# Kernel tuning notes

Hardware: AMD Instinct MI355X
Metric: run time of the kernel (lower is better)

The kernel has to match this reference:

```python
import jax, jax.numpy as jnp
import numpy as np

D = 768
HEAD_DIM = 64
NHEADS = D // HEAD_DIM
B, S = 2, 4096


def setup_inputs() -> dict:
    key = jax.random.key(0)
    ks = jax.random.split(key, 9)
    std = 1.0 / np.sqrt(D)
    inp = {"x": jax.random.normal(ks[0], (B, S, D), dtype=jnp.float32)}
    for i, name in enumerate(["Wq", "Wk", "Wv", "Wo"]):
        inp[name + "_w"] = jax.random.uniform(ks[1 + 2 * i], (D, D), dtype=jnp.float32, minval=-std, maxval=std)
        inp[name + "_b"] = jax.random.uniform(ks[2 + 2 * i], (D,), dtype=jnp.float32, minval=-std, maxval=std)
    return inp


def reference(x, Wq_w, Wq_b, Wk_w, Wk_b, Wv_w, Wv_b, Wo_w, Wo_b):
    b, s, d = x.shape
    # nn.Linear: y = x @ W.T + b
    q = x @ Wq_w.T + Wq_b
    k = x @ Wk_w.T + Wk_b
    v = x @ Wv_w.T + Wv_b
    # [B, H, S, hd]
    q = q.reshape(b, s, NHEADS, HEAD_DIM).transpose(0, 2, 1, 3)
    k = k.reshape(b, s, NHEADS, HEAD_DIM).transpose(0, 2, 1, 3)
    v = v.reshape(b, s, NHEADS, HEAD_DIM).transpose(0, 2, 1, 3)
    scale = jnp.sqrt(jnp.asarray(HEAD_DIM, dtype=q.dtype))
    logits = jnp.einsum('bhqd,bhkd->bhqk', q, k) / scale  # [B,H,S,S]
    causal_mask = jnp.triu(jnp.ones((s, s), dtype=bool), k=1)
    logits = jnp.where(causal_mask, -jnp.inf, logits)
    a = jax.nn.softmax(logits, axis=-1)
    preout = jnp.einsum('bhqk,bhkd->bhqd', a, v)
    preout = preout.transpose(0, 2, 1, 3).reshape(b, s, d)
    return preout @ Wo_w.T + Wo_b
```

## Files before the change

kernel.cpp:

```cpp
#include <hip/hip_runtime.h>

typedef unsigned short u16;
typedef unsigned int u32;
typedef __bf16 bf16_t;
typedef bf16_t bf16x8 __attribute__((ext_vector_type(8)));
typedef float f32x4 __attribute__((ext_vector_type(4)));
typedef float f32x16 __attribute__((ext_vector_type(16)));

#define DM 768
#define HD 64
#define NH 12
#define NB 2
#define SEQ 4096
#define MR (NB * SEQ)

#define SCL2E_F (0.125f * 1.44269504088896340736f)

__device__ __forceinline__ u16 f2bf(float f) {
  union { float f; u32 u; } v;
  v.f = f;
  u32 r = v.u + 0x7FFFu + ((v.u >> 16) & 1u);
  return (u16)(r >> 16);
}

__device__ __forceinline__ u32 cvtpk(float a, float b) {
  u32 r;
  asm("v_cvt_pk_bf16_f32 %0, %1, %2" : "=v"(r) : "v"(a), "v"(b));
  return r;
}

__device__ __forceinline__ bf16x8 ldb8(const u16* p) {
  return *reinterpret_cast<const bf16x8*>(p);
}

__device__ __forceinline__ f32x4 mfma16(bf16x8 a, bf16x8 b, f32x4 c) {
  return __builtin_amdgcn_mfma_f32_16x16x32_bf16(a, b, c, 0, 0, 0);
}

__device__ __forceinline__ f32x16 mfma32(bf16x8 a, bf16x8 b, f32x16 c) {
  return __builtin_amdgcn_mfma_f32_32x32x16_bf16(a, b, c, 0, 0, 0);
}

#define GLDS16(g, l)                                              \
  __builtin_amdgcn_global_load_lds(                               \
      (const __attribute__((address_space(1))) void*)(g),         \
      (__attribute__((address_space(3))) void*)(l), 16, 0, 0)

__global__ __launch_bounds__(256) void cvt_kernel(const float* __restrict__ src,
                                                  u16* __restrict__ dst, int n8) {
  int i = blockIdx.x * 256 + threadIdx.x;
  if (i >= n8) return;
  const float4* s = reinterpret_cast<const float4*>(src) + (size_t)i * 2;
  float4 a = s[0], b = s[1];
  union { u16 u[8]; uint4 v; } o;
  o.u[0] = f2bf(a.x); o.u[1] = f2bf(a.y); o.u[2] = f2bf(a.z); o.u[3] = f2bf(a.w);
  o.u[4] = f2bf(b.x); o.u[5] = f2bf(b.y); o.u[6] = f2bf(b.z); o.u[7] = f2bf(b.w);
  reinterpret_cast<uint4*>(dst)[i] = o.v;
}

__global__ __launch_bounds__(256) void cvt_w_kernel(const float* __restrict__ w0,
                                                    const float* __restrict__ w1,
                                                    const float* __restrict__ w2,
                                                    const float* __restrict__ w3,
                                                    u16* __restrict__ dst) {
  const float* src = (blockIdx.y == 0) ? w0 : (blockIdx.y == 1) ? w1
                   : (blockIdx.y == 2) ? w2 : w3;
  u16* d = dst + (size_t)blockIdx.y * DM * DM;
  int i = blockIdx.x * 256 + threadIdx.x;
  const float4* s = reinterpret_cast<const float4*>(src) + (size_t)i * 2;
  float4 a = s[0], b = s[1];
  union { u16 u[8]; uint4 v; } o;
  o.u[0] = f2bf(a.x); o.u[1] = f2bf(a.y); o.u[2] = f2bf(a.z); o.u[3] = f2bf(a.w);
  o.u[4] = f2bf(b.x); o.u[5] = f2bf(b.y); o.u[6] = f2bf(b.z); o.u[7] = f2bf(b.w);
  reinterpret_cast<uint4*>(d)[i] = o.v;
}

__global__ __launch_bounds__(256) void gemm_qkv_kernel(
    const u16* __restrict__ A, const u16* __restrict__ Wall,
    const float* __restrict__ b0, const float* __restrict__ b1,
    const float* __restrict__ b2, u16* __restrict__ O) {
  __shared__ __align__(16) u16 As[128 * 32];
  __shared__ __align__(16) u16 Bs[128 * 32];

  const int tid = threadIdx.x;
  const int w = tid >> 6, lane = tid & 63;
  const int l16 = lane & 15, lg = lane >> 4;
  const int wm = w >> 1, wn = w & 1;

  const int m0 = blockIdx.x * 128;
  const int n0 = blockIdx.y * 128;
  const int z = blockIdx.z;

  const u16* W = Wall + (size_t)z * DM * DM;
  const float* bias = (z == 0) ? b0 : ((z == 1) ? b1 : b2);
  u16* oz = O + (size_t)z * MR * DM;
  const float qscale = (z == 0) ? SCL2E_F : 1.f;

  f32x4 acc[4][4];
#pragma unroll
  for (int i = 0; i < 4; ++i)
#pragma unroll
    for (int j = 0; j < 4; ++j) {
      acc[i][j][0] = 0.f; acc[i][j][1] = 0.f;
      acc[i][j][2] = 0.f; acc[i][j][3] = 0.f;
    }

  for (int k0 = 0; k0 < DM; k0 += 32) {
#pragma unroll
    for (int i = 0; i < 2; ++i) {
      const int c = (w * 2 + i) * 64 + lane;
      const int m = c >> 2, kc = c & 3;
      GLDS16(A + (size_t)(m0 + m) * DM + (k0 + kc * 8),
             As + (size_t)(w * 2 + i) * 512);
      GLDS16(W + (size_t)(n0 + m) * DM + (k0 + kc * 8),
             Bs + (size_t)(w * 2 + i) * 512);
    }
    __syncthreads();
    bf16x8 af[4], bfv[4];
#pragma unroll
    for (int i = 0; i < 4; ++i)
      af[i] = ldb8(As + (wm * 64 + i * 16 + l16) * 32 + lg * 8);
#pragma unroll
    for (int j = 0; j < 4; ++j)
      bfv[j] = ldb8(Bs + (wn * 64 + j * 16 + l16) * 32 + lg * 8);
#pragma unroll
    for (int i = 0; i < 4; ++i)
#pragma unroll
      for (int j = 0; j < 4; ++j)
        acc[i][j] = mfma16(af[i], bfv[j], acc[i][j]);
    __syncthreads();
  }

#pragma unroll
  for (int i = 0; i < 4; ++i) {
    const int gm = m0 + wm * 64 + i * 16 + lg * 4;
    const int bb = gm >> 12;
    const int ss = gm & (SEQ - 1);
#pragma unroll
    for (int j = 0; j < 4; ++j) {
      const int gn = n0 + wn * 64 + j * 16 + l16;
      const int hh = gn >> 6, dd = gn & (HD - 1);
      const float bv = bias[gn];
      if (z == 2) {
        union { u16 u[4]; uint2 v; } pk;
#pragma unroll
        for (int r = 0; r < 4; ++r) pk.u[r] = f2bf(acc[i][j][r] + bv);
        *reinterpret_cast<uint2*>(
            oz + ((size_t)(bb * NH + hh) * HD + dd) * SEQ + ss) = pk.v;
      } else {
        u16* op = oz + ((size_t)(bb * NH + hh) * SEQ + ss) * HD + dd;
#pragma unroll
        for (int r = 0; r < 4; ++r)
          op[(size_t)r * HD] = f2bf((acc[i][j][r] + bv) * qscale);
      }
    }
  }
}

__global__ __launch_bounds__(256) void gemm_out_kernel(
    const u16* __restrict__ A, const u16* __restrict__ W,
    const float* __restrict__ bias, float* __restrict__ Out) {
  __shared__ __align__(16) u16 As[128 * 32];
  __shared__ __align__(16) u16 Bs[128 * 32];

  const int tid = threadIdx.x;
  const int w = tid >> 6, lane = tid & 63;
  const int l16 = lane & 15, lg = lane >> 4;
  const int wm = w >> 1, wn = w & 1;

  const int m0 = blockIdx.x * 128;
  const int n0 = blockIdx.y * 128;

  f32x4 acc[4][4];
#pragma unroll
  for (int i = 0; i < 4; ++i)
#pragma unroll
    for (int j = 0; j < 4; ++j) {
      acc[i][j][0] = 0.f; acc[i][j][1] = 0.f;
      acc[i][j][2] = 0.f; acc[i][j][3] = 0.f;
    }

  for (int k0 = 0; k0 < DM; k0 += 32) {
#pragma unroll
    for (int i = 0; i < 2; ++i) {
      const int c = (w * 2 + i) * 64 + lane;
      const int m = c >> 2, kc = c & 3;
      GLDS16(A + (size_t)(m0 + m) * DM + (k0 + kc * 8),
             As + (size_t)(w * 2 + i) * 512);
      GLDS16(W + (size_t)(n0 + m) * DM + (k0 + kc * 8),
             Bs + (size_t)(w * 2 + i) * 512);
    }
    __syncthreads();
    bf16x8 af[4], bfv[4];
#pragma unroll
    for (int i = 0; i < 4; ++i)
      af[i] = ldb8(As + (wm * 64 + i * 16 + l16) * 32 + lg * 8);
#pragma unroll
    for (int j = 0; j < 4; ++j)
      bfv[j] = ldb8(Bs + (wn * 64 + j * 16 + l16) * 32 + lg * 8);
#pragma unroll
    for (int i = 0; i < 4; ++i)
#pragma unroll
      for (int j = 0; j < 4; ++j)
        acc[i][j] = mfma16(af[i], bfv[j], acc[i][j]);
    __syncthreads();
  }

#pragma unroll
  for (int i = 0; i < 4; ++i) {
    const int gm = m0 + wm * 64 + i * 16 + lg * 4;
#pragma unroll
    for (int j = 0; j < 4; ++j) {
      const int gn = n0 + wn * 64 + j * 16 + l16;
      const float bv = bias[gn];
      float* op = Out + (size_t)gm * DM + gn;
#pragma unroll
      for (int r = 0; r < 4; ++r)
        op[(size_t)r * DM] = acc[i][j][r] + bv;
    }
  }
}

__global__ __launch_bounds__(256) void attn_kernel(
    const u16* __restrict__ Qg, const u16* __restrict__ Kg,
    const u16* __restrict__ VTg, u16* __restrict__ Og) {
  __shared__ __align__(16) u16 Kt[2][64][72];
  __shared__ __align__(16) u16 Vt[2][64][72];

  const int tid = threadIdx.x;
  const int w = tid >> 6, lane = tid & 63;
  const int l32 = lane & 31, hi = lane >> 5;

  const int idx = blockIdx.x;
  const int qt = 31 - (idx / 24);
  const int bh = idx % 24;
  const int bb = bh / NH, hh = bh % NH;

  const u16* Qp = Qg + (size_t)bh * SEQ * HD;
  const u16* Kp = Kg + (size_t)bh * SEQ * HD;
  const u16* VTp = VTg + (size_t)bh * HD * SEQ;

  const int qw0 = qt * 128 + w * 32;
  const int qlane = qw0 + l32;

  bf16x8 qf[4];
#pragma unroll
  for (int c = 0; c < 4; ++c)
    qf[c] = ldb8(Qp + (size_t)qlane * HD + c * 16 + hi * 8);

  f32x16 oacc[2];
#pragma unroll
  for (int db = 0; db < 2; ++db)
#pragma unroll
    for (int r = 0; r < 16; ++r) oacc[db][r] = 0.f;
  float mrun = -__builtin_inff();
  float lsum = 0.f;

  const int srow = tid >> 3;
  const int sc8 = (tid & 7) * 8;

  {
    uint4 a = *reinterpret_cast<const uint4*>(Kp + (size_t)srow * HD + sc8);
    uint4 b = *reinterpret_cast<const uint4*>(
        Kp + (size_t)(srow + 32) * HD + sc8);
    uint4 c = *reinterpret_cast<const uint4*>(
        VTp + (size_t)srow * SEQ + sc8);
    uint4 d = *reinterpret_cast<const uint4*>(
        VTp + (size_t)(srow + 32) * SEQ + sc8);
    *reinterpret_cast<uint4*>(&Kt[0][srow][sc8]) = a;
    *reinterpret_cast<uint4*>(&Kt[0][srow + 32][sc8]) = b;
    *reinterpret_cast<uint4*>(&Vt[0][srow][sc8]) = c;
    *reinterpret_cast<uint4*>(&Vt[0][srow + 32][sc8]) = d;
  }

  const int NT = 2 * qt + 2;
  int cur = 0;
  for (int t = 0; t < NT; ++t) {
    const int kv0 = t * 64;
    const bool pf = (t + 1 < NT);
    uint4 nK0, nK1, nV0, nV1;
    if (pf) {
      const int nk = kv0 + 64;
      nK0 = *reinterpret_cast<const uint4*>(
          Kp + (size_t)(nk + srow) * HD + sc8);
      nK1 = *reinterpret_cast<const uint4*>(
          Kp + (size_t)(nk + srow + 32) * HD + sc8);
      nV0 = *reinterpret_cast<const uint4*>(
          VTp + (size_t)srow * SEQ + nk + sc8);
      nV1 = *reinterpret_cast<const uint4*>(
          VTp + (size_t)(srow + 32) * SEQ + nk + sc8);
    }
    __syncthreads();

    const bool active = (kv0 <= qw0 + 31);
    f32x16 st[2];
    if (active) {
      __builtin_amdgcn_s_setprio(1);
#pragma unroll
      for (int b = 0; b < 2; ++b) {
#pragma unroll
        for (int r = 0; r < 16; ++r) st[b][r] = 0.f;
#pragma unroll
        for (int c = 0; c < 4; ++c) {
          bf16x8 kf = ldb8(&Kt[cur][b * 32 + l32][c * 16 + hi * 8]);
          st[b] = mfma32(kf, qf[c], st[b]);
        }
      }
      __builtin_amdgcn_s_setprio(0);

      if (kv0 + 63 > qw0) {
#pragma unroll
        for (int b = 0; b < 2; ++b)
#pragma unroll
          for (int r = 0; r < 16; ++r) {
            const int kvi = kv0 + b * 32 + (r & 3) + 8 * (r >> 2) + 4 * hi;
            if (kvi > qlane) st[b][r] = -__builtin_inff();
          }
      }

      float mx[8];
#pragma unroll
      for (int r = 0; r < 8; ++r)
        mx[r] = fmaxf(fmaxf(st[0][r], st[0][r + 8]),
                      fmaxf(st[1][r], st[1][r + 8]));
#pragma unroll
      for (int r = 0; r < 4; ++r) mx[r] = fmaxf(mx[r], mx[r + 4]);
      mx[0] = fmaxf(mx[0], mx[2]);
      mx[1] = fmaxf(mx[1], mx[3]);
      float mt = fmaxf(mx[0], mx[1]);
      mt = fmaxf(mt, __shfl_xor(mt, 32));

      if (__any(mt > mrun + 8.f)) {
        const float mnew = fmaxf(mrun, mt);
        const float corr = exp2f(mrun - mnew);
        lsum *= corr;
#pragma unroll
        for (int db = 0; db < 2; ++db)
#pragma unroll
          for (int r = 0; r < 16; ++r) oacc[db][r] *= corr;
        mrun = mnew;
      }

#pragma unroll
      for (int r = 0; r < 16; ++r) {
        st[0][r] = exp2f(st[0][r] - mrun);
        st[1][r] = exp2f(st[1][r] - mrun);
      }
      float sm[8];
#pragma unroll
      for (int r = 0; r < 8; ++r)
        sm[r] = (st[0][r] + st[0][r + 8]) + (st[1][r] + st[1][r + 8]);
#pragma unroll
      for (int r = 0; r < 4; ++r) sm[r] += sm[r + 4];
      lsum += (sm[0] + sm[2]) + (sm[1] + sm[3]);
    }

    if (pf) {
      *reinterpret_cast<uint4*>(&Kt[cur ^ 1][srow][sc8]) = nK0;
      *reinterpret_cast<uint4*>(&Kt[cur ^ 1][srow + 32][sc8]) = nK1;
      *reinterpret_cast<uint4*>(&Vt[cur ^ 1][srow][sc8]) = nV0;
      *reinterpret_cast<uint4*>(&Vt[cur ^ 1][srow + 32][sc8]) = nV1;
    }

    if (active) {
#pragma unroll
      for (int b = 0; b < 2; ++b) {
#pragma unroll
        for (int h = 0; h < 2; ++h) {
          u32 a0 = cvtpk(st[b][h * 8 + 0], st[b][h * 8 + 1]);
          u32 a1 = cvtpk(st[b][h * 8 + 2], st[b][h * 8 + 3]);
          u32 a2 = cvtpk(st[b][h * 8 + 4], st[b][h * 8 + 5]);
          u32 a3 = cvtpk(st[b][h * 8 + 6], st[b][h * 8 + 7]);
          const u32 p0 = (u32)__shfl_xor((int)a0, 32);
          const u32 p1 = (u32)__shfl_xor((int)a1, 32);
          const u32 p2 = (u32)__shfl_xor((int)a2, 32);
          const u32 p3 = (u32)__shfl_xor((int)a3, 32);
          union { u32 w[4]; bf16x8 v; } pb;
          pb.w[0] = hi ? p2 : a0;
          pb.w[1] = hi ? p3 : a1;
          pb.w[2] = hi ? a2 : p0;
          pb.w[3] = hi ? a3 : p1;
          const int c = 2 * b + h;
          __builtin_amdgcn_s_setprio(1);
#pragma unroll
          for (int db = 0; db < 2; ++db) {
            bf16x8 vf = ldb8(&Vt[cur][db * 32 + l32][c * 16 + hi * 8]);
            oacc[db] = mfma32(vf, pb.v, oacc[db]);
          }
          __builtin_amdgcn_s_setprio(0);
        }
      }
    }
    cur ^= 1;
  }

  const float ltot = lsum + __shfl_xor(lsum, 32);
  const float linv = 1.f / ltot;

  u16* Op = Og + ((size_t)bb * SEQ + qlane) * DM + hh * HD;
#pragma unroll
  for (int db = 0; db < 2; ++db)
#pragma unroll
    for (int r = 0; r < 16; r += 2) {
      const int d = db * 32 + (r & 3) + 8 * (r >> 2) + 4 * hi;
      u32 pk = cvtpk(oacc[db][r] * linv, oacc[db][r + 1] * linv);
      *reinterpret_cast<u32*>(Op + d) = pk;
    }
}

extern "C" void kernel_launch(void* const* d_in, const int* in_sizes, int n_in,
                              void* d_out, int out_size, void* d_ws,
                              size_t ws_size, hipStream_t stream) {
  const float* x  = (const float*)d_in[0];
  const float* Wq = (const float*)d_in[1];
  const float* bq = (const float*)d_in[2];
  const float* Wk = (const float*)d_in[3];
  const float* bk = (const float*)d_in[4];
  const float* Wv = (const float*)d_in[5];
  const float* bv = (const float*)d_in[6];
  const float* Wo = (const float*)d_in[7];
  const float* bo = (const float*)d_in[8];
  float* out = (float*)d_out;

  u16* xb   = (u16*)d_ws;
  u16* Wall = xb + (size_t)MR * DM;
  u16* QKV  = Wall + (size_t)4 * DM * DM;
  u16* PRE  = QKV + (size_t)3 * MR * DM;

  cvt_kernel<<<dim3(MR * DM / 8 / 256), 256, 0, stream>>>(x, xb, MR * DM / 8);
  cvt_w_kernel<<<dim3(DM * DM / 8 / 256, 4), 256, 0, stream>>>(Wq, Wk, Wv, Wo,
                                                               Wall);
  gemm_qkv_kernel<<<dim3(MR / 128, DM / 128, 3), 256, 0, stream>>>(
      xb, Wall, bq, bk, bv, QKV);
  attn_kernel<<<dim3(768), 256, 0, stream>>>(
      QKV, QKV + (size_t)MR * DM, QKV + (size_t)2 * MR * DM, PRE);
  gemm_out_kernel<<<dim3(MR / 128, DM / 128), 256, 0, stream>>>(
      PRE, Wall + (size_t)3 * DM * DM, bo, out);
}
```

Before: 213.3 us.

## Fold running max into MFMA accumulator init, use permlane32 swap and packed adds

The attention inner loop now seeds the QK^T MFMA accumulator with the negated running max (cneg), so the max subtraction happens inside the MFMA and the per-element subtract before exp2 goes away in the common no-rescale case. The bf16 P-fragment exchange between wave halves uses v_permlane32_swap instead of four ds-swizzle shuffles plus selects, and the row-sum reduction uses packed f32 adds. This trims VALU and LDS-permute work on the softmax critical path. In exchange it adds a branch with two exp paths and depends on cneg staying consistent with the rescaling logic.

```diff
diff --git a/kernel.cpp b/kernel.cpp
--- a/kernel.cpp
+++ b/kernel.cpp
@@ -4,6 +4,7 @@
 typedef unsigned int u32;
 typedef __bf16 bf16_t;
 typedef bf16_t bf16x8 __attribute__((ext_vector_type(8)));
+typedef float f32x2 __attribute__((ext_vector_type(2)));
 typedef float f32x4 __attribute__((ext_vector_type(4)));
 typedef float f32x16 __attribute__((ext_vector_type(16)));
 
@@ -26,6 +27,16 @@
 __device__ __forceinline__ u32 cvtpk(float a, float b) {
   u32 r;
   asm("v_cvt_pk_bf16_f32 %0, %1, %2" : "=v"(r) : "v"(a), "v"(b));
+  return r;
+}
+
+__device__ __forceinline__ void pl32swap(u32& a, u32& b) {
+  asm volatile("v_permlane32_swap_b32 %0, %1" : "+v"(a), "+v"(b));
+}
+
+__device__ __forceinline__ f32x2 pkadd(f32x2 a, f32x2 b) {
+  f32x2 r;
+  asm("v_pk_add_f32 %0, %1, %2" : "=v"(r) : "v"(a), "v"(b));
   return r;
 }
 
@@ -249,11 +260,13 @@
     qf[c] = ldb8(Qp + (size_t)qlane * HD + c * 16 + hi * 8);
 
   f32x16 oacc[2];
+  f32x16 cneg;
+#pragma unroll
+  for (int r = 0; r < 16; ++r) cneg[r] = 0.f;
 #pragma unroll
   for (int db = 0; db < 2; ++db)
 #pragma unroll
     for (int r = 0; r < 16; ++r) oacc[db][r] = 0.f;
-  float mrun = -__builtin_inff();
   float lsum = 0.f;
 
   const int srow = tid >> 3;
@@ -298,10 +311,12 @@
       __builtin_amdgcn_s_setprio(1);
 #pragma unroll
       for (int b = 0; b < 2; ++b) {
-#pragma unroll
-        for (int r = 0; r < 16; ++r) st[b][r] = 0.f;
-#pragma unroll
-        for (int c = 0; c < 4; ++c) {
+        {
+          bf16x8 kf = ldb8(&Kt[cur][b * 32 + l32][hi * 8]);
+          st[b] = mfma32(kf, qf[0], cneg);
+        }
+#pragma unroll
+        for (int c = 1; c < 4; ++c) {
           bf16x8 kf = ldb8(&Kt[cur][b * 32 + l32][c * 16 + hi * 8]);
           st[b] = mfma32(kf, qf[c], st[b]);
         }
@@ -325,34 +340,45 @@
                       fmaxf(st[1][r], st[1][r + 8]));
 #pragma unroll
       for (int r = 0; r < 4; ++r) mx[r] = fmaxf(mx[r], mx[r + 4]);
-      mx[0] = fmaxf(mx[0], mx[2]);
-      mx[1] = fmaxf(mx[1], mx[3]);
-      float mt = fmaxf(mx[0], mx[1]);
+      float mt = fmaxf(fmaxf(mx[0], mx[1]), fmaxf(mx[2], mx[3]));
       mt = fmaxf(mt, __shfl_xor(mt, 32));
 
-      if (__any(mt > mrun + 8.f)) {
-        const float mnew = fmaxf(mrun, mt);
-        const float corr = exp2f(mrun - mnew);
+      if (__any(mt > 8.f)) {
+        const float dm = fmaxf(mt, 0.f);
+        const float corr = exp2f(-dm);
         lsum *= corr;
 #pragma unroll
         for (int db = 0; db < 2; ++db)
 #pragma unroll
           for (int r = 0; r < 16; ++r) oacc[db][r] *= corr;
-        mrun = mnew;
-      }
-
-#pragma unroll
-      for (int r = 0; r < 16; ++r) {
-        st[0][r] = exp2f(st[0][r] - mrun);
-        st[1][r] = exp2f(st[1][r] - mrun);
-      }
-      float sm[8];
-#pragma unroll
-      for (int r = 0; r < 8; ++r)
-        sm[r] = (st[0][r] + st[0][r + 8]) + (st[1][r] + st[1][r + 8]);
-#pragma unroll
-      for (int r = 0; r < 4; ++r) sm[r] += sm[r + 4];
-      lsum += (sm[0] + sm[2]) + (sm[1] + sm[3]);
+#pragma unroll
+        for (int r = 0; r < 16; ++r) cneg[r] -= dm;
+#pragma unroll
+        for (int r = 0; r < 16; ++r) {
+          st[0][r] = exp2f(st[0][r] - dm);
+          st[1][r] = exp2f(st[1][r] - dm);
+        }
+      } else {
+#pragma unroll
+        for (int r = 0; r < 16; ++r) {
+          st[0][r] = exp2f(st[0][r]);
+          st[1][r] = exp2f(st[1][r]);
+        }
+      }
+
+      {
+        const f32x2* h0 = reinterpret_cast<const f32x2*>(&st[0]);
+        const f32x2* h1 = reinterpret_cast<const f32x2*>(&st[1]);
+        f32x2 t2[8];
+#pragma unroll
+        for (int i = 0; i < 8; ++i) t2[i] = pkadd(h0[i], h1[i]);
+#pragma unroll
+        for (int i = 0; i < 4; ++i) t2[i] = pkadd(t2[i], t2[i + 4]);
+        t2[0] = pkadd(t2[0], t2[2]);
+        t2[1] = pkadd(t2[1], t2[3]);
+        t2[0] = pkadd(t2[0], t2[1]);
+        lsum += t2[0][0] + t2[0][1];
+      }
     }
 
     if (pf) {
@@ -371,15 +397,10 @@
           u32 a1 = cvtpk(st[b][h * 8 + 2], st[b][h * 8 + 3]);
           u32 a2 = cvtpk(st[b][h * 8 + 4], st[b][h * 8 + 5]);
           u32 a3 = cvtpk(st[b][h * 8 + 6], st[b][h * 8 + 7]);
-          const u32 p0 = (u32)__shfl_xor((int)a0, 32);
-          const u32 p1 = (u32)__shfl_xor((int)a1, 32);
-          const u32 p2 = (u32)__shfl_xor((int)a2, 32);
-          const u32 p3 = (u32)__shfl_xor((int)a3, 32);
+          pl32swap(a0, a2);
+          pl32swap(a1, a3);
           union { u32 w[4]; bf16x8 v; } pb;
-          pb.w[0] = hi ? p2 : a0;
-          pb.w[1] = hi ? p3 : a1;
-          pb.w[2] = hi ? a2 : p0;
-          pb.w[3] = hi ? a3 : p1;
+          pb.w[0] = a0; pb.w[1] = a1; pb.w[2] = a2; pb.w[3] = a3;
           const int c = 2 * b + h;
           __builtin_amdgcn_s_setprio(1);
 #pragma unroll
```

Result: slower. 271.7 us (+27.4%).
